# Optimization experiments

Measured on AMD Instinct MI355X. Metric: run time of the kernel, lower is better.

## Reference

```python
import jax, jax.numpy as jnp
import numpy as np
import math

NUM_HEADS = 16
D_KV = 64
D_MODEL = 1024
NUM_BUCKETS = 32
MAX_DISTANCE = 128
SEQ = 2048
BATCH = 2


def _relative_position_bucket(relative_position):
    # bidirectional T5 bucketing
    num_buckets = NUM_BUCKETS // 2  # 16
    buckets = (relative_position > 0).astype(jnp.int32) * num_buckets
    rp = jnp.abs(relative_position)
    max_exact = num_buckets // 2  # 8
    is_small = rp < max_exact
    rp_safe = jnp.maximum(rp, 1)  # avoid log(0); masked by is_small anyway
    rp_large = max_exact + (
        jnp.log(rp_safe.astype(jnp.float32) / max_exact)
        / math.log(MAX_DISTANCE / max_exact)
        * (num_buckets - max_exact)
    ).astype(jnp.int32)
    rp_large = jnp.minimum(rp_large, num_buckets - 1)
    return buckets + jnp.where(is_small, rp, rp_large)


def _position_bias(rel_bias_table, q_len, k_len):
    ctx = jnp.arange(q_len)[:, None]
    mem = jnp.arange(k_len)[None, :]
    buckets = _relative_position_bucket(mem - ctx)  # (q,k)
    vals = rel_bias_table[buckets]  # (q,k,h)
    return jnp.transpose(vals, (2, 0, 1))[None]  # (1,h,q,k)


def setup_inputs() -> dict:
    key = jax.random.key(0)
    ks = jax.random.split(key, 6)
    s = 1.0 / math.sqrt(D_MODEL)
    return {
        "hidden_states": jax.random.normal(ks[0], (BATCH, SEQ, D_MODEL), jnp.float32),
        "Wq": jax.random.normal(ks[1], (D_MODEL, NUM_HEADS * D_KV), jnp.float32) * s,
        "Wk": jax.random.normal(ks[2], (D_MODEL, NUM_HEADS * D_KV), jnp.float32) * s,
        "Wv": jax.random.normal(ks[3], (D_MODEL, NUM_HEADS * D_KV), jnp.float32) * s,
        "Wo": jax.random.normal(ks[4], (NUM_HEADS * D_KV, D_MODEL), jnp.float32) * s,
        "rel_bias_table": jax.random.normal(ks[5], (NUM_BUCKETS, NUM_HEADS), jnp.float32),
    }


def reference(hidden_states, Wq, Wk, Wv, Wo, rel_bias_table):
    b, s, _ = hidden_states.shape
    q = (hidden_states @ Wq).reshape(b, s, NUM_HEADS, D_KV).transpose(0, 2, 1, 3)
    k = (hidden_states @ Wk).reshape(b, s, NUM_HEADS, D_KV).transpose(0, 2, 1, 3)
    v = (hidden_states @ Wv).reshape(b, s, NUM_HEADS, D_KV).transpose(0, 2, 1, 3)
    # T5: NO query scaling, additive relative-position bias
    scores = jnp.einsum("bhqd,bhkd->bhqk", q, k) + _position_bias(rel_bias_table, s, s)
    attn = jax.nn.softmax(scores, axis=-1)  # dropout is identity in eval
    out = jnp.einsum("bhqk,bhkd->bhqd", attn, v)
    out = out.transpose(0, 2, 1, 3).reshape(b, s, NUM_HEADS * D_KV)
    return out @ Wo
```

## Files before the change

### kernel.cpp

```cpp
#include <hip/hip_runtime.h>
#include <hip/hip_bf16.h>
#include <math.h>

#define NUM_HEADS 16
#define D_KV 64
#define D_MODEL 1024
#define SEQ 2048
#define BATCH 2
#define LOG2E 1.4426950408889634f

using bf16x8 = __attribute__((ext_vector_type(8))) short;
using bf16x4 = __attribute__((ext_vector_type(4))) short;
using f32x4  = __attribute__((ext_vector_type(4))) float;

__device__ inline unsigned short f2bf(float f) {
  union { float f; unsigned int i; } v; v.f = f;
  unsigned int u = v.i;
  return (unsigned short)((u + 0x7FFFu + ((u >> 16) & 1u)) >> 16);
}
__device__ inline unsigned short f2bf_fast(float f) {
  union { float f; unsigned int i; } v; v.f = f;
  return (unsigned short)((v.i + 0x8000u) >> 16);
}

#if __has_builtin(__builtin_amdgcn_exp2f)
#define EXP2(x) __builtin_amdgcn_exp2f(x)
#else
#define EXP2(x) __expf((x) * 0.6931471805599453f)
#endif

__device__ inline unsigned int pk_bf16(float a, float b) {
#if __has_builtin(__builtin_amdgcn_cvt_pk_bf16_f32)
  auto v = __builtin_amdgcn_cvt_pk_bf16_f32(a, b);
  unsigned int u; __builtin_memcpy(&u, &v, 4);
  return u;
#else
  return ((unsigned int)f2bf_fast(b) << 16) | f2bf_fast(a);
#endif
}

__device__ inline void gld_lds16(const unsigned short* g, unsigned short* l) {
  __builtin_amdgcn_global_load_lds(
      (const __attribute__((address_space(1))) unsigned int*)g,
      (__attribute__((address_space(3))) unsigned int*)l, 16, 0, 0);
}

__global__ __launch_bounds__(256) void prep_kernel(const float* __restrict__ X,
                                                   const float* __restrict__ W0,
                                                   const float* __restrict__ W1,
                                                   const float* __restrict__ W2,
                                                   const float* __restrict__ W3,
                                                   const float* __restrict__ tbl,
                                                   unsigned short* __restrict__ xbf,
                                                   unsigned short* __restrict__ wt,
                                                   float* __restrict__ biasF) {
  __shared__ __align__(16) unsigned short T[64][72];
  int bid = blockIdx.x;
  int t = threadIdx.x;
  if (bid < 2048) {
    int i = (bid * 256 + t) * 8;
    __align__(16) unsigned short tmp[8];
#pragma unroll
    for (int e = 0; e < 8; e++) tmp[e] = f2bf(X[i + e]);
    *(uint4*)&xbf[i] = *(uint4*)tmp;
  } else if (bid < 3072) {
    int rem = bid - 2048;
    int z = rem >> 8, tid = rem & 255;
    const float* in = (z == 0) ? W0 : (z == 1) ? W1 : (z == 2) ? W2 : W3;
    unsigned short* o = wt + (long)z * 1048576;
    int r0 = (tid & 15) * 64, c0 = (tid >> 4) * 64;
#pragma unroll
    for (int i = 0; i < 2; i++) {
      int c = t + 256 * i; int r = c >> 3, k8 = (c & 7) * 8;
      const float* src = &in[(long)(r0 + r) * 1024 + c0 + k8];
      __align__(16) unsigned short tmp[8];
#pragma unroll
      for (int e = 0; e < 8; e++) tmp[e] = f2bf(src[e]);
      *(uint4*)&T[r][k8] = *(uint4*)tmp;
    }
    __syncthreads();
#pragma unroll
    for (int i = 0; i < 2; i++) {
      int c = t + 256 * i; int r = c >> 3, k8 = (c & 7) * 8;
      __align__(16) unsigned short tmp[8];
#pragma unroll
      for (int e = 0; e < 8; e++) tmp[e] = T[k8 + e][r];
      *(uint4*)&o[(long)(c0 + r) * 1024 + r0 + k8] = *(uint4*)tmp;
    }
  } else {
    int h = bid - 3072;
#pragma unroll
    for (int ii = 0; ii < 16; ii++) {
      int idx = t + 256 * ii;
      if (idx >= 4095) break;
      int rel = idx - 2047;
      int bucket = (rel > 0) ? 16 : 0;
      int rp = rel < 0 ? -rel : rel;
      int add;
      if (rp < 8) add = rp;
      else {
        int rl = 8 + (int)(logf((float)rp * 0.125f) / logf(16.0f) * 8.0f);
        add = rl < 15 ? rl : 15;
      }
      bucket += add;
      biasF[h * 4096 + idx] = tbl[bucket * 16 + h] * LOG2E;
    }
  }
}

__global__ __launch_bounds__(256) void gemm_kernel(const unsigned short* __restrict__ X,
                                                   const unsigned short* __restrict__ Wt,
                                                   unsigned short* __restrict__ out_b,
                                                   unsigned short* __restrict__ out_vt) {
  __shared__ __align__(16) unsigned short SMEM[128 * 136];
  unsigned short* As = SMEM;
  unsigned short* Bs = SMEM + 8192;
  const int K = 1024;
  int bid0 = blockIdx.x + (blockIdx.y << 5) + (blockIdx.z << 8);
  int swz  = (bid0 & 7) * 96 + (bid0 >> 3);
  int m0 = (swz & 31) * 128;
  int n0 = ((swz >> 5) & 7) * 128;
  int zz = swz >> 8;
  const unsigned short* W = Wt + (long)zz * 1048576;
  unsigned short* outq = out_b + (long)zz * 4194304;
  float scale = (zz == 0) ? LOG2E : 1.0f;
  int t = threadIdx.x;
  int w = t >> 6, l = t & 63;
  int wr = (w >> 1) * 64, wc = (w & 1) * 64;
  int lr = l & 15, lq = l >> 4;
  f32x4 acc[4][4];
#pragma unroll
  for (int i = 0; i < 4; i++)
#pragma unroll
    for (int j = 0; j < 4; j++) acc[i][j] = (f32x4){0.f, 0.f, 0.f, 0.f};

  auto STAGE = [&](int buf, int k0) {
    unsigned short* A = As + buf * 4096;
    unsigned short* B = Bs + buf * 4096;
#pragma unroll
    for (int i = 0; i < 2; i++) {
      int c = t + 256 * i;
      int r = c >> 2, kc = (c & 3) * 8;
      gld_lds16(&X[(long)(m0 + r) * K + k0 + kc], &A[c * 8]);
      gld_lds16(&W[(long)(n0 + r) * K + k0 + kc], &B[c * 8]);
    }
  };

  STAGE(0, 0);
  for (int k0 = 0; k0 < K; k0 += 32) {
    int cur = (k0 >> 5) & 1;
    bool more = k0 + 32 < K;
    if (more) {
      STAGE(cur ^ 1, k0 + 32);
      asm volatile("s_waitcnt vmcnt(4)" ::: "memory");
    } else {
      asm volatile("s_waitcnt vmcnt(0)" ::: "memory");
    }
    __builtin_amdgcn_s_barrier();
    __builtin_amdgcn_sched_barrier(0);
    const unsigned short* Ab = As + cur * 4096;
    const unsigned short* Bb = Bs + cur * 4096;
    bf16x8 a[4], b[4];
#pragma unroll
    for (int mi = 0; mi < 4; mi++) a[mi] = *(const bf16x8*)&Ab[(wr + mi * 16 + lr) * 32 + lq * 8];
#pragma unroll
    for (int ni = 0; ni < 4; ni++) b[ni] = *(const bf16x8*)&Bb[(wc + ni * 16 + lr) * 32 + lq * 8];
#pragma unroll
    for (int mi = 0; mi < 4; mi++)
#pragma unroll
      for (int ni = 0; ni < 4; ni++)
        acc[mi][ni] = __builtin_amdgcn_mfma_f32_16x16x32_bf16(a[mi], b[ni], acc[mi][ni], 0, 0, 0);
    asm volatile("s_waitcnt lgkmcnt(0)" ::: "memory");
    __builtin_amdgcn_s_barrier();
    __builtin_amdgcn_sched_barrier(0);
  }

  if (zz == 2) {
    unsigned short* Cs = SMEM;
#pragma unroll
    for (int mi = 0; mi < 4; mi++)
#pragma unroll
      for (int ni = 0; ni < 4; ni++) {
        int nl = wc + ni * 16 + lr;
        int ml = wr + mi * 16 + lq * 4;
        unsigned int s0 = pk_bf16(acc[mi][ni][0], acc[mi][ni][1]);
        unsigned int s1 = pk_bf16(acc[mi][ni][2], acc[mi][ni][3]);
        *(uint2*)&Cs[nl * 136 + ml] = (uint2){s0, s1};
      }
    __syncthreads();
    int b2 = m0 >> 11, sbase = m0 & 2047;
#pragma unroll
    for (int i = 0; i < 8; i++) {
      int c = t + 256 * i;
      int row = c >> 4, ch = c & 15;
      uint4 v = *(const uint4*)&Cs[row * 136 + ch * 8];
      int n = n0 + row, h = n >> 6, d = n & 63;
      *(uint4*)&out_vt[(((long)(b2 * 16 + h) * 64 + d) << 11) + sbase + ch * 8] = v;
    }
  } else {
    unsigned short* Cs = SMEM;
#pragma unroll
    for (int mi = 0; mi < 4; mi++)
#pragma unroll
      for (int ni = 0; ni < 4; ni++)
#pragma unroll
        for (int r = 0; r < 4; r++)
          Cs[(wr + mi * 16 + lq * 4 + r) * 136 + wc + ni * 16 + lr] = f2bf(acc[mi][ni][r] * scale);
    __syncthreads();
    int b2 = m0 >> 11, sbase = m0 & 2047;
#pragma unroll
    for (int i = 0; i < 8; i++) {
      int c = t + 256 * i;
      int row = c >> 4, ch = c & 15;
      uint4 v = *(const uint4*)&Cs[row * 136 + ch * 8];
      int n = n0 + ch * 8, h = n >> 6, d = n & 63;
      *(uint4*)&outq[((long)(b2 * 16 + h) * 2048 + sbase + row) * 64 + d] = v;
    }
  }
}

__global__ __launch_bounds__(256) void ogemm_kernel(const unsigned short* __restrict__ X,
                                                    const unsigned short* __restrict__ W,
                                                    float* __restrict__ out) {
  __shared__ __align__(16) unsigned char SMEM[57344];
  unsigned short* As = (unsigned short*)SMEM;
  unsigned short* Bs = As + 16384;
  float* Csf = (float*)SMEM;
  const int K = 1024;
  int bid0 = blockIdx.x + (blockIdx.y << 5);
  int swz  = (bid0 & 7) * 64 + (bid0 >> 3);
  int m0 = (swz & 31) * 128;
  int n0 = (swz >> 5) * 64;
  int t = threadIdx.x;
  int w = t >> 6, l = t & 63;
  int wr = (w >> 1) * 64, wc = (w & 1) * 32;
  int lr = l & 15, lq = l >> 4;
  f32x4 acc[4][2];
#pragma unroll
  for (int i = 0; i < 4; i++)
#pragma unroll
    for (int j = 0; j < 2; j++) acc[i][j] = (f32x4){0.f, 0.f, 0.f, 0.f};

  auto STAGE = [&](int buf, int k0) {
    unsigned short* A = As + buf * 8192;
    unsigned short* B = Bs + buf * 4096;
#pragma unroll
    for (int i = 0; i < 4; i++) {
      int c = t + 256 * i;
      int p = c >> 9, r = (c >> 2) & 127, kc = (c & 3) * 8;
      gld_lds16(&X[(long)(m0 + r) * K + k0 + p * 32 + kc], &A[c * 8]);
    }
#pragma unroll
    for (int i = 0; i < 2; i++) {
      int c = t + 256 * i;
      int p = c >> 8, r = (c >> 2) & 63, kc = (c & 3) * 8;
      gld_lds16(&W[(long)(n0 + r) * K + k0 + p * 32 + kc], &B[c * 8]);
    }
  };

  STAGE(0, 0);
  for (int k0 = 0; k0 < K; k0 += 64) {
    int cur = (k0 >> 6) & 1;
    bool more = k0 + 64 < K;
    if (more) {
      STAGE(cur ^ 1, k0 + 64);
      asm volatile("s_waitcnt vmcnt(6)" ::: "memory");
    } else {
      asm volatile("s_waitcnt vmcnt(0)" ::: "memory");
    }
    __builtin_amdgcn_s_barrier();
    __builtin_amdgcn_sched_barrier(0);
    const unsigned short* Ab = As + cur * 8192;
    const unsigned short* Bb = Bs + cur * 4096;
    bf16x8 a[4][2], b[2][2];
#pragma unroll
    for (int ks = 0; ks < 2; ks++) {
#pragma unroll
      for (int mi = 0; mi < 4; mi++) a[mi][ks] = *(const bf16x8*)&Ab[ks * 4096 + (wr + mi * 16 + lr) * 32 + lq * 8];
#pragma unroll
      for (int ni = 0; ni < 2; ni++) b[ni][ks] = *(const bf16x8*)&Bb[ks * 2048 + (wc + ni * 16 + lr) * 32 + lq * 8];
    }
#pragma unroll
    for (int ks = 0; ks < 2; ks++)
#pragma unroll
      for (int mi = 0; mi < 4; mi++)
#pragma unroll
        for (int ni = 0; ni < 2; ni++)
          acc[mi][ni] = __builtin_amdgcn_mfma_f32_16x16x32_bf16(a[mi][ks], b[ni][ks], acc[mi][ni], 0, 0, 0);
    asm volatile("s_waitcnt lgkmcnt(0)" ::: "memory");
    __builtin_amdgcn_s_barrier();
    __builtin_amdgcn_sched_barrier(0);
  }

#pragma unroll
  for (int p = 0; p < 2; p++) {
    if (p) __syncthreads();
    if ((w >> 1) == p) {
#pragma unroll
      for (int mi = 0; mi < 4; mi++)
#pragma unroll
        for (int ni = 0; ni < 2; ni++)
#pragma unroll
          for (int r = 0; r < 4; r++)
            Csf[(mi * 16 + lq * 4 + r) * 68 + wc + ni * 16 + lr] = acc[mi][ni][r];
    }
    __syncthreads();
#pragma unroll
    for (int i = 0; i < 4; i++) {
      int c = t + 256 * i;
      int row = c >> 4, ch = c & 15;
      float4 v = *(const float4*)&Csf[row * 68 + ch * 4];
      *(float4*)&out[(long)(m0 + p * 64 + row) * 1024 + n0 + ch * 4] = v;
    }
  }
}

__global__ __launch_bounds__(512) void attn_kernel(const unsigned short* __restrict__ Q,
                                                   const unsigned short* __restrict__ Km,
                                                   const unsigned short* __restrict__ Vt,
                                                   const float* __restrict__ biasF,
                                                   unsigned short* __restrict__ O) {
  __shared__ __align__(16) unsigned short KV[4][4608];
  int q0 = blockIdx.x * 128;
  int bh = blockIdx.y;
  int b_ = bh >> 4, h = bh & 15;
  const unsigned short* Qb = Q  + (long)bh * SEQ * 64;
  const unsigned short* Kb = Km + (long)bh * SEQ * 64;
  const unsigned short* Vb = Vt + (long)bh * 64 * SEQ;
  const float* btabF = biasF + h * 4096;
  int t = threadIdx.x;
  int w = t >> 6, l = t & 63;
  int g = w >> 2, wg = w & 3;
  int lr = l & 15, lq = l >> 4;
  int qw = wg * 32;

  float bL = btabF[0], bH = btabF[4094];

  const float* bgl = btabF + (2047 - q0 - qw - lr + lq * 4);

  bf16x8 aq[2][2];
#pragma unroll
  for (int qt = 0; qt < 2; qt++)
#pragma unroll
    for (int ks = 0; ks < 2; ks++)
      aq[qt][ks] = *(const bf16x8*)&Qb[(long)(q0 + qw + qt * 16 + lr) * 64 + ks * 32 + lq * 8];

  int rs = t >> 3, fs = (t & 7) * 8;

  int ktpS = (fs >> 5) & 1;
  int q2 = (fs >> 3) & 3;
  int caS = ktpS * 4 + (q2 & 1) * 2;
  int offS = (q2 >> 1) * 4;
  int vo1 = rs * 72 + caS * 8 + offS;
  int vo2 = vo1 + 8;

  uint4 kpa = *(const uint4*)&Kb[(long)rs * 64 + fs];
  uint4 kpb = *(const uint4*)&Kb[(long)(64 + rs) * 64 + fs];
  uint4 vpa = *(const uint4*)&Vb[(long)rs * SEQ + fs];
  uint4 vpb = *(const uint4*)&Vb[(long)rs * SEQ + 64 + fs];
  *(uint4*)&KV[0][rs * 72 + fs] = kpa;
  *(uint4*)&KV[1][rs * 72 + fs] = kpb;
  *(uint2*)&KV[2][vo1] = (uint2){vpa.x, vpa.y};
  *(uint2*)&KV[2][vo2] = (uint2){vpa.z, vpa.w};
  *(uint2*)&KV[3][vo1] = (uint2){vpb.x, vpb.y};
  *(uint2*)&KV[3][vo2] = (uint2){vpb.z, vpb.w};

  f32x4 accO[4][2];
  float rsum[2] = {0.f, 0.f};
#pragma unroll
  for (int qt = 0; qt < 2; qt++)
#pragma unroll
    for (int dt = 0; dt < 4; dt++) accO[dt][qt] = (f32x4){0.f, 0.f, 0.f, 0.f};

  for (int i = 0; i < 16; i++) {
    __syncthreads();
    int k0 = (2 * i + g) * 64;
    bool more = i < 15;

    float bblf[5][4];
    int dq = k0 - q0;
    if (dq >= 218 || dq <= -154) {
      float bc = (dq >= 218) ? bH : bL;
#pragma unroll
      for (int m = 0; m < 5; m++)
#pragma unroll
        for (int j = 0; j < 4; j++) bblf[m][j] = bc;
    } else {
      const float* bb = bgl + (k0 - 16);
#pragma unroll
      for (int m = 0; m < 5; m++)
#pragma unroll
        for (int j = 0; j < 4; j++) bblf[m][j] = bb[16 * m + j];
    }

    bf16x8 bk[4][2];
#pragma unroll
    for (int kt = 0; kt < 4; kt++)
#pragma unroll
      for (int ks = 0; ks < 2; ks++)
        bk[kt][ks] = *(const bf16x8*)&KV[g][(kt * 16 + lr) * 72 + ks * 32 + lq * 8];

    if (more) {
      const unsigned short* Kn = Kb + (long)(2 * i + 2) * 64 * 64;
      const unsigned short* Vn = Vb + (2 * i + 2) * 64;
      kpa = *(const uint4*)&Kn[(long)rs * 64 + fs];
      kpb = *(const uint4*)&Kn[(long)(64 + rs) * 64 + fs];
      vpa = *(const uint4*)&Vn[(long)rs * SEQ + fs];
      vpb = *(const uint4*)&Vn[(long)rs * SEQ + 64 + fs];
    }

    f32x4 sacc[4][2];
#pragma unroll
    for (int kt = 0; kt < 4; kt++)
#pragma unroll
      for (int qt = 0; qt < 2; qt++) sacc[kt][qt] = (f32x4){0.f, 0.f, 0.f, 0.f};
#pragma unroll
    for (int ks = 0; ks < 2; ks++)
#pragma unroll
      for (int kt = 0; kt < 4; kt++)
#pragma unroll
        for (int qt = 0; qt < 2; qt++)
          sacc[kt][qt] = __builtin_amdgcn_mfma_f32_16x16x32_bf16(bk[kt][ks], aq[qt][ks], sacc[kt][qt], 0, 0, 0);

#pragma unroll
    for (int ktp = 0; ktp < 2; ktp++) {
      bf16x8 va8[4];
#pragma unroll
      for (int dt = 0; dt < 4; dt++)
        va8[dt] = *(const bf16x8*)&KV[2 + g][(dt * 16 + lr) * 72 + (ktp * 4 + lq) * 8];
#pragma unroll
      for (int qt = 0; qt < 2; qt++) {
        unsigned int u[4];
#pragma unroll
        for (int kth = 0; kth < 2; kth++) {
          int kt = ktp * 2 + kth;
          int blk = kt - qt + 1;
          float p0 = EXP2(sacc[kt][qt][0] + bblf[blk][0]);
          float p1 = EXP2(sacc[kt][qt][1] + bblf[blk][1]);
          float p2 = EXP2(sacc[kt][qt][2] + bblf[blk][2]);
          float p3 = EXP2(sacc[kt][qt][3] + bblf[blk][3]);
          rsum[qt] += (p0 + p1) + (p2 + p3);
          u[kth * 2]     = pk_bf16(p0, p1);
          u[kth * 2 + 1] = pk_bf16(p2, p3);
        }
        union { unsigned int uu[4]; bf16x8 v; } pbu;
        pbu.uu[0] = u[0]; pbu.uu[1] = u[1]; pbu.uu[2] = u[2]; pbu.uu[3] = u[3];
#pragma unroll
        for (int dt = 0; dt < 4; dt++)
          accO[dt][qt] = __builtin_amdgcn_mfma_f32_16x16x32_bf16(va8[dt], pbu.v, accO[dt][qt], 0, 0, 0);
      }
    }

    __syncthreads();
    if (more) {
      *(uint4*)&KV[0][rs * 72 + fs] = kpa;
      *(uint4*)&KV[1][rs * 72 + fs] = kpb;
      *(uint2*)&KV[2][vo1] = (uint2){vpa.x, vpa.y};
      *(uint2*)&KV[2][vo2] = (uint2){vpa.z, vpa.w};
      *(uint2*)&KV[3][vo1] = (uint2){vpb.x, vpb.y};
      *(uint2*)&KV[3][vo2] = (uint2){vpb.z, vpb.w};
    }
  }

#pragma unroll
  for (int qt = 0; qt < 2; qt++) {
    rsum[qt] += __shfl_xor(rsum[qt], 16);
    rsum[qt] += __shfl_xor(rsum[qt], 32);
  }

  float* mrg = (float*)&KV[0][0];
  int slot = (wg * 64 + l) * 34;
  if (g == 1) {
    float2* mp = (float2*)&mrg[slot];
    int j = 0;
#pragma unroll
    for (int dt = 0; dt < 4; dt++)
#pragma unroll
      for (int qt = 0; qt < 2; qt++) {
        mp[j++] = (float2){accO[dt][qt][0], accO[dt][qt][1]};
        mp[j++] = (float2){accO[dt][qt][2], accO[dt][qt][3]};
      }
    mp[16] = (float2){rsum[0], rsum[1]};
  }
  __syncthreads();
  if (g == 0) {
    const float2* mp = (const float2*)&mrg[slot];
    int j = 0;
#pragma unroll
    for (int dt = 0; dt < 4; dt++)
#pragma unroll
      for (int qt = 0; qt < 2; qt++) {
        float2 a = mp[j++], b2 = mp[j++];
        accO[dt][qt][0] += a.x;  accO[dt][qt][1] += a.y;
        accO[dt][qt][2] += b2.x; accO[dt][qt][3] += b2.y;
      }
    float2 ls = mp[16];
    float rl0 = 1.0f / (rsum[0] + ls.x);
    float rl1 = 1.0f / (rsum[1] + ls.y);
#pragma unroll
    for (int qt = 0; qt < 2; qt++) {
      float rl = qt ? rl1 : rl0;
      int q = q0 + qw + qt * 16 + lr;
#pragma unroll
      for (int dt = 0; dt < 4; dt++) {
        unsigned int s0 = ((unsigned int)f2bf(accO[dt][qt][1] * rl) << 16) | f2bf(accO[dt][qt][0] * rl);
        unsigned int s1 = ((unsigned int)f2bf(accO[dt][qt][3] * rl) << 16) | f2bf(accO[dt][qt][2] * rl);
        *(uint2*)&O[((long)(b_ * SEQ + q)) * 1024 + h * 64 + dt * 16 + lq * 4] = (uint2){s0, s1};
      }
    }
  }
}

extern "C" void kernel_launch(void* const* d_in, const int* in_sizes, int n_in,
                              void* d_out, int out_size, void* d_ws, size_t ws_size,
                              hipStream_t stream) {
  const float* X   = (const float*)d_in[0];
  const float* Wq  = (const float*)d_in[1];
  const float* Wk  = (const float*)d_in[2];
  const float* Wv  = (const float*)d_in[3];
  const float* Wo  = (const float*)d_in[4];
  const float* tbl = (const float*)d_in[5];

  unsigned short* wt    = (unsigned short*)d_ws;
  unsigned short* xbf   = wt + 4 * 1048576;
  unsigned short* q_ws  = xbf + 4194304;
  unsigned short* k_ws  = q_ws + 4194304;
  unsigned short* vt_ws = k_ws + 4194304;
  float* biasF = (float*)(vt_ws + 4194304);
  unsigned short* o_ws  = xbf;

  prep_kernel<<<3088, 256, 0, stream>>>(X, Wq, Wk, Wv, Wo, tbl, xbf, wt, biasF);
  gemm_kernel<<<dim3(32, 8, 3), 256, 0, stream>>>(xbf, wt, q_ws, vt_ws);
  attn_kernel<<<dim3(16, 32), 512, 0, stream>>>(q_ws, k_ws, vt_ws, biasF, o_ws);
  ogemm_kernel<<<dim3(32, 16), 256, 0, stream>>>(o_ws, wt + 3 * 1048576, (float*)d_out);
}
```

Measured before the change: 197.7 us.

## Load V fragments directly from global into registers, bypassing LDS staging

The V tile is no longer staged through shared memory with a permuted layout. Each wave now loads its MFMA V operands straight from global memory as two 4-element vectors per fragment and concatenates them in registers. This cuts LDS stores, reads and footprint for V, and frees it from the prefetch and barrier path. The cost is many small, poorly coalesced global loads that are issued at the start of each iteration, so their latency is exposed before the PV MFMAs. The V data is also re-read redundantly by the four waves in a group rather than shared through LDS.

```diff
diff --git a/kernel.cpp b/kernel.cpp
--- a/kernel.cpp
+++ b/kernel.cpp
@@ -320,7 +320,8 @@
                                                    const unsigned short* __restrict__ Vt,
                                                    const float* __restrict__ biasF,
                                                    unsigned short* __restrict__ O) {
-  __shared__ __align__(16) unsigned short KV[4][4608];
+  __shared__ __align__(16) unsigned char SMEMA[36864];
+  unsigned short (*KS)[4608] = (unsigned short(*)[4608])SMEMA;
   int q0 = blockIdx.x * 128;
   int bh = blockIdx.y;
   int b_ = bh >> 4, h = bh & 15;
@@ -347,23 +348,10 @@
 
   int rs = t >> 3, fs = (t & 7) * 8;
 
-  int ktpS = (fs >> 5) & 1;
-  int q2 = (fs >> 3) & 3;
-  int caS = ktpS * 4 + (q2 & 1) * 2;
-  int offS = (q2 >> 1) * 4;
-  int vo1 = rs * 72 + caS * 8 + offS;
-  int vo2 = vo1 + 8;
-
   uint4 kpa = *(const uint4*)&Kb[(long)rs * 64 + fs];
   uint4 kpb = *(const uint4*)&Kb[(long)(64 + rs) * 64 + fs];
-  uint4 vpa = *(const uint4*)&Vb[(long)rs * SEQ + fs];
-  uint4 vpb = *(const uint4*)&Vb[(long)rs * SEQ + 64 + fs];
-  *(uint4*)&KV[0][rs * 72 + fs] = kpa;
-  *(uint4*)&KV[1][rs * 72 + fs] = kpb;
-  *(uint2*)&KV[2][vo1] = (uint2){vpa.x, vpa.y};
-  *(uint2*)&KV[2][vo2] = (uint2){vpa.z, vpa.w};
-  *(uint2*)&KV[3][vo1] = (uint2){vpb.x, vpb.y};
-  *(uint2*)&KV[3][vo2] = (uint2){vpb.z, vpb.w};
+  *(uint4*)&KS[0][rs * 72 + fs] = kpa;
+  *(uint4*)&KS[1][rs * 72 + fs] = kpb;
 
   f32x4 accO[4][2];
   float rsum[2] = {0.f, 0.f};
@@ -377,6 +365,16 @@
     int k0 = (2 * i + g) * 64;
     bool more = i < 15;
 
+    bf16x4 vglo[2][4], vghi[2][4];
+#pragma unroll
+    for (int ktp = 0; ktp < 2; ktp++)
+#pragma unroll
+      for (int dt = 0; dt < 4; dt++) {
+        const unsigned short* vp = &Vb[(long)(dt * 16 + lr) * SEQ + k0 + ktp * 32 + lq * 4];
+        vglo[ktp][dt] = *(const bf16x4*)vp;
+        vghi[ktp][dt] = *(const bf16x4*)(vp + 16);
+      }
+
     float bblf[5][4];
     int dq = k0 - q0;
     if (dq >= 218 || dq <= -154) {
@@ -398,15 +396,12 @@
     for (int kt = 0; kt < 4; kt++)
 #pragma unroll
       for (int ks = 0; ks < 2; ks++)
-        bk[kt][ks] = *(const bf16x8*)&KV[g][(kt * 16 + lr) * 72 + ks * 32 + lq * 8];
+        bk[kt][ks] = *(const bf16x8*)&KS[g][(kt * 16 + lr) * 72 + ks * 32 + lq * 8];
 
     if (more) {
       const unsigned short* Kn = Kb + (long)(2 * i + 2) * 64 * 64;
-      const unsigned short* Vn = Vb + (2 * i + 2) * 64;
       kpa = *(const uint4*)&Kn[(long)rs * 64 + fs];
       kpb = *(const uint4*)&Kn[(long)(64 + rs) * 64 + fs];
-      vpa = *(const uint4*)&Vn[(long)rs * SEQ + fs];
-      vpb = *(const uint4*)&Vn[(long)rs * SEQ + 64 + fs];
     }
 
     f32x4 sacc[4][2];
@@ -427,7 +422,7 @@
       bf16x8 va8[4];
 #pragma unroll
       for (int dt = 0; dt < 4; dt++)
-        va8[dt] = *(const bf16x8*)&KV[2 + g][(dt * 16 + lr) * 72 + (ktp * 4 + lq) * 8];
+        va8[dt] = __builtin_shufflevector(vglo[ktp][dt], vghi[ktp][dt], 0, 1, 2, 3, 4, 5, 6, 7);
 #pragma unroll
       for (int qt = 0; qt < 2; qt++) {
         unsigned int u[4];
@@ -453,12 +448,8 @@
 
     __syncthreads();
     if (more) {
-      *(uint4*)&KV[0][rs * 72 + fs] = kpa;
-      *(uint4*)&KV[1][rs * 72 + fs] = kpb;
-      *(uint2*)&KV[2][vo1] = (uint2){vpa.x, vpa.y};
-      *(uint2*)&KV[2][vo2] = (uint2){vpa.z, vpa.w};
-      *(uint2*)&KV[3][vo1] = (uint2){vpb.x, vpb.y};
-      *(uint2*)&KV[3][vo2] = (uint2){vpb.z, vpb.w};
+      *(uint4*)&KS[0][rs * 72 + fs] = kpa;
+      *(uint4*)&KS[1][rs * 72 + fs] = kpb;
     }
   }
 
@@ -468,7 +459,7 @@
     rsum[qt] += __shfl_xor(rsum[qt], 32);
   }
 
-  float* mrg = (float*)&KV[0][0];
+  float* mrg = (float*)SMEMA;
   int slot = (wg * 64 + l) * 34;
   if (g == 1) {
     float2* mp = (float2*)&mrg[slot];
```

New measurement: 297.9 us. 1.51x slower.
